# Kernel optimization log

Measured on AMD Instinct MI355X. Metric: run time of the kernel, lower is better.

Reference implementation:

```python
import jax, jax.numpy as jnp
import numpy as np

N, N2, N3 = 40000, 20000, 10000
E, E2, E3 = 640000, 320000, 160000
HEADS = 4
F_IN = 5


def _glorot(k, shape):
    lim = float(np.sqrt(6.0 / (shape[0] + shape[-1])))
    return jax.random.uniform(k, shape, jnp.float32, -lim, lim)


def setup_inputs() -> dict:
    key = jax.random.key(0)
    ks = jax.random.split(key, 40)
    inp = {}
    inp["x"] = jax.random.normal(ks[0], (N, F_IN), jnp.float32)
    inp["edge_index"] = jax.random.randint(ks[1], (2, E), 0, N)
    inp["edge_index2"] = jax.random.randint(ks[2], (2, E2), 0, N2)
    inp["edge_index3"] = jax.random.randint(ks[3], (2, E3), 0, N3)
    # graclus-style cluster maps; constructed surjective so no cluster is empty
    inp["cluster1"] = jax.random.permutation(ks[4], jnp.arange(N) % N2)
    inp["cluster2"] = jax.random.permutation(ks[5], jnp.arange(N2) % N3)
    dims = [(F_IN, 16), (16, 32), (32, 64), (64, 32), (64, 16)]
    i = 6
    for idx, (fi, fo) in enumerate(dims, 1):
        inp[f"cW{idx}"] = _glorot(ks[i], (fi, HEADS * fo)); i += 1
        inp[f"cU{idx}"] = _glorot(ks[i], (fi, HEADS)); i += 1
        inp[f"cc{idx}"] = jnp.zeros((HEADS,), jnp.float32)
        inp[f"cb{idx}"] = jnp.zeros((fo,), jnp.float32)
    inp["l1W"] = _glorot(ks[i], (32, 256)); i += 1
    inp["l1b"] = jnp.zeros((256,), jnp.float32)
    inp["l2W"] = _glorot(ks[i], (256, 6890)); i += 1
    inp["l2b"] = jnp.zeros((6890,), jnp.float32)
    inp["oW"] = _glorot(ks[i], (6890, 1)); i += 1
    inp["ob"] = jnp.zeros((1,), jnp.float32)
    return inp


def feast_conv(x, ei, W, U, c, b, n, fo):
    """PyG FeaStConv: self-loops, per-edge head-softmax attention, mean aggregation."""
    sl = jnp.arange(n)
    src = jnp.concatenate([ei[0], sl])  # message sources (x_j)
    dst = jnp.concatenate([ei[1], sl])  # aggregation targets (x_i)
    xs, xd = x[src], x[dst]
    q = jax.nn.softmax((xs - xd) @ U + c, axis=-1)          # [E+n, H]
    m = (xs @ W).reshape(-1, HEADS, fo)                      # [E+n, H, fo]
    msg = jnp.einsum('eh,eho->eo', q, m)                     # [E+n, fo]
    agg = jax.ops.segment_sum(msg, dst, num_segments=n)
    cnt = jax.ops.segment_sum(jnp.ones((dst.shape[0],), x.dtype), dst, num_segments=n)
    return agg / cnt[:, None] + b


def _forward(x, edge_index, edge_index2, edge_index3, cluster1, cluster2, p):
    x1 = jax.nn.relu(feast_conv(x, edge_index, p["cW1"], p["cU1"], p["cc1"], p["cb1"], N, 16))
    x2 = jax.ops.segment_max(x1, cluster1, num_segments=N2)                     # graclus max_pool
    x2 = jax.nn.relu(feast_conv(x2, edge_index2, p["cW2"], p["cU2"], p["cc2"], p["cb2"], N2, 32))
    x3 = jax.ops.segment_max(x2, cluster2, num_segments=N3)
    x3 = jax.nn.relu(feast_conv(x3, edge_index3, p["cW3"], p["cU3"], p["cc3"], p["cb3"], N3, 64))
    x3 = jax.nn.relu(feast_conv(x3, edge_index3, p["cW4"], p["cU4"], p["cc4"], p["cb4"], N3, 32))
    x3 = jnp.concatenate([x2, x3[cluster2]], axis=1)                            # [N2, 64] unpool+skip
    x3 = jax.nn.relu(feast_conv(x3, edge_index2, p["cW5"], p["cU5"], p["cc5"], p["cb5"], N2, 16))
    h = jnp.concatenate([x1, x3[cluster1]], axis=1)                             # [N, 32]
    h = jax.nn.relu(h @ p["l1W"] + p["l1b"])
    h = jax.nn.relu(h @ p["l2W"] + p["l2b"])                                   # [N, 6890]
    return jax.nn.sigmoid(h @ p["oW"] + p["ob"])                                # [N, 1]


def reference(x, edge_index, edge_index2, edge_index3, cluster1, cluster2,
              cW1, cU1, cc1, cb1, cW2, cU2, cc2, cb2, cW3, cU3, cc3, cb3,
              cW4, cU4, cc4, cb4, cW5, cU5, cc5, cb5, l1W, l1b, l2W, l2b, oW, ob):
    p = dict(cW1=cW1, cU1=cU1, cc1=cc1, cb1=cb1, cW2=cW2, cU2=cU2, cc2=cc2, cb2=cb2,
             cW3=cW3, cU3=cU3, cc3=cc3, cb3=cb3, cW4=cW4, cU4=cU4, cc4=cc4, cb4=cb4,
             cW5=cW5, cU5=cU5, cc5=cc5, cb5=cb5, l1W=l1W, l1b=l1b, l2W=l2W, l2b=l2b,
             oW=oW, ob=ob)
    return _forward(x, edge_index, edge_index2, edge_index3, cluster1, cluster2, p)
```

## Files before the change

### kernel.cpp

```cpp
#include <hip/hip_runtime.h>
#include <math.h>

#define N1  40000
#define NN2 20000
#define NN3 10000
#define EE1 640000
#define EE2 320000
#define EE3 160000
#define JPAD 6912
#define JREAL 6890
#define NTILE 432
#define CSPLIT 8
#define TPB (NTILE/CSPLIT)
#define NSTG (TPB/2)
#define NROWP 40192
#define NGRP 628
#define CAP 64

typedef __attribute__((ext_vector_type(8))) short short8;
typedef __attribute__((ext_vector_type(4))) float f32x4;

__device__ inline unsigned short f2bf(float f) {
  unsigned u = __float_as_uint(f);
  u += 0x7FFF + ((u >> 16) & 1);
  return (unsigned short)(u >> 16);
}

__global__ void k_matmulWU(const float* __restrict__ Xa, int fa,
                           const float* __restrict__ Xb, int fb,
                           const int* __restrict__ map,
                           const float* __restrict__ W, const float* __restrict__ U,
                           float* __restrict__ xW, float* __restrict__ xU,
                           int n, int co) {
  int ct = co + 4;
  int idx = blockIdx.x * 256 + threadIdx.x;
  if (idx >= n * ct) return;
  int row = idx / ct, col = idx - row * ct;
  const float* M;
  int stride;
  if (col < co) { M = W + col; stride = co; }
  else          { M = U + (col - co); stride = 4; }
  float s = 0.f;
  const float* ar = Xa + (size_t)row * fa;
  for (int k = 0; k < fa; ++k) s = fmaf(ar[k], M[(size_t)k * stride], s);
  if (Xb) {
    const float* br = Xb + (size_t)map[row] * fb;
    for (int k = 0; k < fb; ++k) s = fmaf(br[k], M[(size_t)(fa + k) * stride], s);
  }
  if (col < co) xW[(size_t)row * co + col] = s;
  else          xU[(size_t)row * 4 + (col - co)] = s;
}

__global__ void k_xU(const float* __restrict__ xin, const float* __restrict__ U,
                     float* __restrict__ xu, int n, int ci) {
  int idx = blockIdx.x * 256 + threadIdx.x;
  if (idx >= n * 4) return;
  int h = idx & 3, d = idx >> 2;
  const float* xr = xin + (size_t)d * ci;
  float s = 0.f;
  for (int k = 0; k < ci; ++k) s = fmaf(xr[k], U[k * 4 + h], s);
  xu[idx] = s;
}

__global__ void k_pad8(const float* __restrict__ x, float* __restrict__ x8) {
  int idx = blockIdx.x * 256 + threadIdx.x;
  if (idx >= N1 * 8) return;
  int d = idx >> 3, k = idx & 7;
  x8[idx] = (k < 5) ? x[d * 5 + k] : 0.f;
}

__global__ void k_build3(const int* __restrict__ ei1, const int* __restrict__ ei2,
                         const int* __restrict__ ei3,
                         int* __restrict__ c1, int* __restrict__ c2, int* __restrict__ c3,
                         int* __restrict__ s1, int* __restrict__ s2, int* __restrict__ s3) {
  int e = blockIdx.x * 256 + threadIdx.x;
  const int* ei; int* cnt; int* sl; int E;
  if (e < EE1) { ei = ei1; cnt = c1; sl = s1; E = EE1; }
  else {
    e -= EE1;
    if (e < EE2) { ei = ei2; cnt = c2; sl = s2; E = EE2; }
    else {
      e -= EE2;
      if (e >= EE3) return;
      ei = ei3; cnt = c3; sl = s3; E = EE3;
    }
  }
  int s = ei[e], d = ei[E + e];
  int pos = atomicAdd(&cnt[d], 1);
  if (pos < CAP) sl[(size_t)d * CAP + pos] = s;
}

__global__ void k_aggX(const int* __restrict__ cnt, const int* __restrict__ slots,
                       const float* __restrict__ xU, const f32x4* __restrict__ xin4,
                       int stride4, const float* __restrict__ c,
                       f32x4* __restrict__ agg4, int n, int ci4) {
  int idx = blockIdx.x * 256 + threadIdx.x;
  if (idx >= n * ci4 * 4) return;
  const int sp = idx & 3;
  int t = idx >> 2;
  const int cg = t % ci4, d = t / ci4;
  const float c0 = c[0], c1 = c[1], c2 = c[2], c3 = c[3];
  const f32x4 xd = ((const f32x4*)xU)[d];
  const int deg = min(cnt[d], CAP);
  const int jlo = (deg * sp) >> 2, jhi = (deg * (sp + 1)) >> 2;
  const int* sl = slots + (size_t)d * CAP;
  f32x4 acc[4];
#pragma unroll
  for (int e = 0; e < 4; ++e) acc[e] = (f32x4){0.f, 0.f, 0.f, 0.f};
  int j = jlo;
  for (; j + 2 <= jhi; j += 2) {
    int sA = sl[j], sB = sl[j + 1];
    f32x4 xsA = ((const f32x4*)xU)[sA];
    f32x4 xsB = ((const f32x4*)xU)[sB];
    f32x4 xvA = xin4[(size_t)sA * stride4 + cg];
    f32x4 xvB = xin4[(size_t)sB * stride4 + cg];
    float lA0 = xsA[0] - xd[0] + c0, lA1 = xsA[1] - xd[1] + c1;
    float lA2 = xsA[2] - xd[2] + c2, lA3 = xsA[3] - xd[3] + c3;
    float mxA = fmaxf(fmaxf(lA0, lA1), fmaxf(lA2, lA3));
    float qA0 = __expf(lA0 - mxA), qA1 = __expf(lA1 - mxA);
    float qA2 = __expf(lA2 - mxA), qA3 = __expf(lA3 - mxA);
    float ivA = 1.f / (qA0 + qA1 + qA2 + qA3);
    f32x4 qA = (f32x4){qA0 * ivA, qA1 * ivA, qA2 * ivA, qA3 * ivA};
    float lB0 = xsB[0] - xd[0] + c0, lB1 = xsB[1] - xd[1] + c1;
    float lB2 = xsB[2] - xd[2] + c2, lB3 = xsB[3] - xd[3] + c3;
    float mxB = fmaxf(fmaxf(lB0, lB1), fmaxf(lB2, lB3));
    float qB0 = __expf(lB0 - mxB), qB1 = __expf(lB1 - mxB);
    float qB2 = __expf(lB2 - mxB), qB3 = __expf(lB3 - mxB);
    float ivB = 1.f / (qB0 + qB1 + qB2 + qB3);
    f32x4 qB = (f32x4){qB0 * ivB, qB1 * ivB, qB2 * ivB, qB3 * ivB};
#pragma unroll
    for (int e = 0; e < 4; ++e) acc[e] += xvA[e] * qA + xvB[e] * qB;
  }
  if (j < jhi) {
    int s = sl[j];
    f32x4 xs = ((const f32x4*)xU)[s];
    f32x4 xv = xin4[(size_t)s * stride4 + cg];
    float l0 = xs[0] - xd[0] + c0, l1 = xs[1] - xd[1] + c1;
    float l2 = xs[2] - xd[2] + c2, l3 = xs[3] - xd[3] + c3;
    float mx = fmaxf(fmaxf(l0, l1), fmaxf(l2, l3));
    float q0 = __expf(l0 - mx), q1 = __expf(l1 - mx);
    float q2 = __expf(l2 - mx), q3 = __expf(l3 - mx);
    float iv = 1.f / (q0 + q1 + q2 + q3);
    f32x4 q = (f32x4){q0 * iv, q1 * iv, q2 * iv, q3 * iv};
#pragma unroll
    for (int e = 0; e < 4; ++e) acc[e] += xv[e] * q;
  }
#pragma unroll
  for (int e = 0; e < 4; ++e)
#pragma unroll
    for (int h = 0; h < 4; ++h) {
      acc[e][h] += __shfl_xor(acc[e][h], 1);
      acc[e][h] += __shfl_xor(acc[e][h], 2);
    }
  if (sp) return;
  {
    float mx = fmaxf(fmaxf(c0, c1), fmaxf(c2, c3));
    float q0 = __expf(c0 - mx), q1 = __expf(c1 - mx);
    float q2 = __expf(c2 - mx), q3 = __expf(c3 - mx);
    float iv = 1.f / (q0 + q1 + q2 + q3);
    f32x4 q = (f32x4){q0 * iv, q1 * iv, q2 * iv, q3 * iv};
    f32x4 xv = xin4[(size_t)d * stride4 + cg];
#pragma unroll
    for (int e = 0; e < 4; ++e) acc[e] += xv[e] * q;
  }
  f32x4* dst = agg4 + (size_t)d * (ci4 * 4) + cg * 4;
#pragma unroll
  for (int e = 0; e < 4; ++e) dst[e] = acc[e];
}

__global__ void k_postW(const f32x4* __restrict__ agg4, int aggstride, int kreal,
                        const float* __restrict__ W, const float* __restrict__ b,
                        const int* __restrict__ cnt, float* __restrict__ outp,
                        int n, int fo,
                        const int* __restrict__ pool_cl, int* __restrict__ pool_out) {
  int idx = blockIdx.x * 256 + threadIdx.x;
  if (idx >= n * fo) return;
  int o = idx % fo, d = idx / fo;
  const int co = 4 * fo;
  const f32x4* ar = agg4 + (size_t)d * aggstride;
  float acc = 0.f;
  for (int k = 0; k < kreal; ++k) {
    f32x4 f = ar[k];
    const float* wr = W + (size_t)k * co + o;
    acc += f[0] * wr[0] + f[1] * wr[fo] + f[2] * wr[2 * fo] + f[3] * wr[3 * fo];
  }
  int deg = min(cnt[d], CAP);
  float v = fmaxf(acc / (float)(deg + 1) + b[o], 0.f);
  outp[idx] = v;
  if (pool_cl)
    atomicMax((int*)&pool_out[(size_t)pool_cl[d] * fo + o], __float_as_int(v));
}

__global__ void k_attagg4(const int* __restrict__ cnt, const int* __restrict__ slots,
                          const float* __restrict__ xU, const float4* __restrict__ xW,
                          const float* __restrict__ c, const float4* __restrict__ b4,
                          float4* __restrict__ outp, int n, int fo4,
                          const int* __restrict__ pool_cl, int* __restrict__ pool_out) {
  int idx = blockIdx.x * 256 + threadIdx.x;
  if (idx >= n * fo4 * 4) return;
  const int sp = idx & 3;
  const int t = idx >> 2;
  const int d = t / fo4, og = t - d * fo4;
  const float c0 = c[0], c1 = c[1], c2 = c[2], c3 = c[3];
  const float4 xd = *(const float4*)&xU[(size_t)d * 4];
  const int deg = min(cnt[d], CAP);
  const int jlo = (deg * sp) >> 2;
  const int jhi = (deg * (sp + 1)) >> 2;
  const int* sl = slots + (size_t)d * CAP;
  float ax = 0.f, ay = 0.f, az = 0.f, aw = 0.f;
  int j = jlo;
  for (; j + 2 <= jhi; j += 2) {
    int sA = sl[j], sB = sl[j + 1];
    float4 xsA = *(const float4*)&xU[(size_t)sA * 4];
    float4 xsB = *(const float4*)&xU[(size_t)sB * 4];
    const float4* mA = xW + (size_t)sA * 4 * fo4 + og;
    const float4* mB = xW + (size_t)sB * 4 * fo4 + og;
    float4 a0 = mA[0], a1 = mA[fo4], a2 = mA[2 * fo4], a3 = mA[3 * fo4];
    float4 e0 = mB[0], e1 = mB[fo4], e2 = mB[2 * fo4], e3 = mB[3 * fo4];
    float lA0 = xsA.x - xd.x + c0, lA1 = xsA.y - xd.y + c1;
    float lA2 = xsA.z - xd.z + c2, lA3 = xsA.w - xd.w + c3;
    float mxA = fmaxf(fmaxf(lA0, lA1), fmaxf(lA2, lA3));
    float qA0 = __expf(lA0 - mxA), qA1 = __expf(lA1 - mxA);
    float qA2 = __expf(lA2 - mxA), qA3 = __expf(lA3 - mxA);
    float ivA = 1.f / (qA0 + qA1 + qA2 + qA3);
    qA0 *= ivA; qA1 *= ivA; qA2 *= ivA; qA3 *= ivA;
    float lB0 = xsB.x - xd.x + c0, lB1 = xsB.y - xd.y + c1;
    float lB2 = xsB.z - xd.z + c2, lB3 = xsB.w - xd.w + c3;
    float mxB = fmaxf(fmaxf(lB0, lB1), fmaxf(lB2, lB3));
    float qB0 = __expf(lB0 - mxB), qB1 = __expf(lB1 - mxB);
    float qB2 = __expf(lB2 - mxB), qB3 = __expf(lB3 - mxB);
    float ivB = 1.f / (qB0 + qB1 + qB2 + qB3);
    qB0 *= ivB; qB1 *= ivB; qB2 *= ivB; qB3 *= ivB;
    ax += qA0 * a0.x + qA1 * a1.x + qA2 * a2.x + qA3 * a3.x
        + qB0 * e0.x + qB1 * e1.x + qB2 * e2.x + qB3 * e3.x;
    ay += qA0 * a0.y + qA1 * a1.y + qA2 * a2.y + qA3 * a3.y
        + qB0 * e0.y + qB1 * e1.y + qB2 * e2.y + qB3 * e3.y;
    az += qA0 * a0.z + qA1 * a1.z + qA2 * a2.z + qA3 * a3.z
        + qB0 * e0.z + qB1 * e1.z + qB2 * e2.z + qB3 * e3.z;
    aw += qA0 * a0.w + qA1 * a1.w + qA2 * a2.w + qA3 * a3.w
        + qB0 * e0.w + qB1 * e1.w + qB2 * e2.w + qB3 * e3.w;
  }
  if (j < jhi) {
    int s = sl[j];
    float4 xs = *(const float4*)&xU[(size_t)s * 4];
    const float4* m = xW + (size_t)s * 4 * fo4 + og;
    float4 m0 = m[0], m1 = m[fo4], m2 = m[2 * fo4], m3 = m[3 * fo4];
    float l0 = xs.x - xd.x + c0, l1 = xs.y - xd.y + c1;
    float l2 = xs.z - xd.z + c2, l3 = xs.w - xd.w + c3;
    float mx = fmaxf(fmaxf(l0, l1), fmaxf(l2, l3));
    float q0 = __expf(l0 - mx), q1 = __expf(l1 - mx);
    float q2 = __expf(l2 - mx), q3 = __expf(l3 - mx);
    float inv = 1.f / (q0 + q1 + q2 + q3);
    q0 *= inv; q1 *= inv; q2 *= inv; q3 *= inv;
    ax += q0 * m0.x + q1 * m1.x + q2 * m2.x + q3 * m3.x;
    ay += q0 * m0.y + q1 * m1.y + q2 * m2.y + q3 * m3.y;
    az += q0 * m0.z + q1 * m1.z + q2 * m2.z + q3 * m3.z;
    aw += q0 * m0.w + q1 * m1.w + q2 * m2.w + q3 * m3.w;
  }
  ax += __shfl_xor(ax, 1); ay += __shfl_xor(ay, 1);
  az += __shfl_xor(az, 1); aw += __shfl_xor(aw, 1);
  ax += __shfl_xor(ax, 2); ay += __shfl_xor(ay, 2);
  az += __shfl_xor(az, 2); aw += __shfl_xor(aw, 2);
  if (sp) return;
  {
    float mx = fmaxf(fmaxf(c0, c1), fmaxf(c2, c3));
    float q0 = __expf(c0 - mx), q1 = __expf(c1 - mx);
    float q2 = __expf(c2 - mx), q3 = __expf(c3 - mx);
    float inv = 1.f / (q0 + q1 + q2 + q3);
    const float4* m = xW + (size_t)d * 4 * fo4 + og;
    float4 m0 = m[0], m1 = m[fo4], m2 = m[2 * fo4], m3 = m[3 * fo4];
    ax += (q0 * m0.x + q1 * m1.x + q2 * m2.x + q3 * m3.x) * inv;
    ay += (q0 * m0.y + q1 * m1.y + q2 * m2.y + q3 * m3.y) * inv;
    az += (q0 * m0.z + q1 * m1.z + q2 * m2.z + q3 * m3.z) * inv;
    aw += (q0 * m0.w + q1 * m1.w + q2 * m2.w + q3 * m3.w) * inv;
  }
  const float inv = 1.f / (float)(deg + 1);
  const float4 bb = b4[og];
  float4 v;
  v.x = fmaxf(ax * inv + bb.x, 0.f);
  v.y = fmaxf(ay * inv + bb.y, 0.f);
  v.z = fmaxf(az * inv + bb.z, 0.f);
  v.w = fmaxf(aw * inv + bb.w, 0.f);
  outp[(size_t)d * fo4 + og] = v;
  if (pool_cl) {
    int* po = pool_out + ((size_t)pool_cl[d] * fo4 + og) * 4;
    atomicMax(&po[0], __float_as_int(v.x));
    atomicMax(&po[1], __float_as_int(v.y));
    atomicMax(&po[2], __float_as_int(v.z));
    atomicMax(&po[3], __float_as_int(v.w));
  }
}

__global__ __launch_bounds__(256) void k_packB(
    const float* __restrict__ l2W, short8* __restrict__ Bp,
    const float* __restrict__ l2b, const float* __restrict__ oW,
    float* __restrict__ l2bp, float* __restrict__ oWp) {
  __shared__ float tile[32][65];
  const int bid = blockIdx.x, tid = threadIdx.x;
  if (bid < 27) {
    int j = bid * 256 + tid;
    l2bp[j] = (j < JREAL) ? l2b[j] : 0.f;
    oWp[j]  = (j < JREAL) ? oW[j]  : 0.f;
  }
  const int kg = bid / 108, jg = bid - kg * 108;
  const int k0 = kg * 32, j0 = jg * 64;
  const int kr = tid >> 6, jc = tid & 63;
  const int j = j0 + jc;
#pragma unroll
  for (int i = 0; i < 8; ++i) {
    int row = kr * 8 + i;
    tile[row][jc] = (j < JREAL) ? l2W[(size_t)(k0 + row) * JREAL + j] : 0.f;
  }
  __syncthreads();
  const int tt = tid >> 6, lane = tid & 63;
  short8 v;
#pragma unroll
  for (int i = 0; i < 8; ++i)
    v[i] = (short)f2bf(tile[((lane >> 4) << 3) + i][tt * 16 + (lane & 15)]);
  Bp[((size_t)(jg * 4 + tt) * 8 + kg) * 64 + lane] = v;
}

__global__ __launch_bounds__(256) void k_packh(
    const float* __restrict__ x1, const float* __restrict__ x5,
    const int* __restrict__ cl1, const float* __restrict__ l1W,
    const float* __restrict__ l1b, short8* __restrict__ Apack) {
  __shared__ float h1s[64][256];
  const int tid = threadIdx.x;
  const int row0 = blockIdx.x * 64;

  float wcol[32];
#pragma unroll
  for (int k = 0; k < 32; ++k) wcol[k] = l1W[k * 256 + tid];
  const float bt = l1b[tid];

  for (int r = 0; r < 64; ++r) {
    const int row = row0 + r;
    float s = bt;
    if (row < N1) {
      const float* a = x1 + (size_t)row * 16;
      const float* b = x5 + (size_t)cl1[row] * 16;
#pragma unroll
      for (int k = 0; k < 16; ++k) s = fmaf(a[k], wcol[k], s);
#pragma unroll
      for (int k = 0; k < 16; ++k) s = fmaf(b[k], wcol[16 + k], s);
    }
    h1s[r][tid ^ ((r & 7) << 3)] = fmaxf(s, 0.f);
  }
  __syncthreads();

#pragma unroll
  for (int j = 0; j < 8; ++j) {
    int s = j * 256 + tid;
    int l = s & 63, ks = (s >> 6) & 7, rb = s >> 9;
    int row = rb * 16 + (l & 15);
    int col0 = (ks * 32 + ((l >> 4) << 3)) ^ ((row & 7) << 3);
    const float* sp = &h1s[row][col0];
    short8 v;
#pragma unroll
    for (int i = 0; i < 8; ++i) v[i] = (short)f2bf(sp[i]);
    Apack[(size_t)blockIdx.x * 2048 + s] = v;
  }
}

__global__ __launch_bounds__(256, 2) void k_final2(
    const short8* __restrict__ Apack, const short8* __restrict__ Bp,
    const float* __restrict__ l2bp, const float* __restrict__ oWp,
    float* __restrict__ zbuf) {
  __shared__ short8 bufs[2][1024];
  const int tid = threadIdx.x, wid = tid >> 6, l = tid & 63;
  const int rg = blockIdx.x >> 3, cg = blockIdx.x & 7;
  const int lm = l & 15, lh = l >> 4;

  short8 af[4][8];
  {
    const short8* ap = Apack + (size_t)(rg * 4 + wid) * 2048 + l;
#pragma unroll
    for (int rb = 0; rb < 4; ++rb)
#pragma unroll
      for (int ks = 0; ks < 8; ++ks) af[rb][ks] = ap[rb * 512 + ks * 64];
  }

  const short8* bsrc = Bp + (size_t)cg * TPB * 512;
  short8 n0 = bsrc[tid], n1 = bsrc[256 + tid], n2 = bsrc[512 + tid], n3 = bsrc[768 + tid];
  bufs[0][tid] = n0; bufs[0][256 + tid] = n1;
  bufs[0][512 + tid] = n2; bufs[0][768 + tid] = n3;
  {
    const short8* p = bsrc + 1024;
    n0 = p[tid]; n1 = p[256 + tid]; n2 = p[512 + tid]; n3 = p[768 + tid];
  }
  asm volatile("s_waitcnt lgkmcnt(0)" ::: "memory");
  __builtin_amdgcn_s_barrier();
  asm volatile("" ::: "memory");

  float zp[4][4];
#pragma unroll
  for (int rb = 0; rb < 4; ++rb)
#pragma unroll
    for (int r = 0; r < 4; ++r) zp[rb][r] = 0.f;

  for (int st = 0; st < NSTG; ++st) {
    const int cur = st & 1;
    if (st + 1 < NSTG) {
      bufs[cur ^ 1][tid] = n0; bufs[cur ^ 1][256 + tid] = n1;
      bufs[cur ^ 1][512 + tid] = n2; bufs[cur ^ 1][768 + tid] = n3;
    }
    if (st + 2 < NSTG) {
      const short8* p = bsrc + (st + 2) * 1024;
      n0 = p[tid]; n1 = p[256 + tid]; n2 = p[512 + tid]; n3 = p[768 + tid];
    }
#pragma unroll
    for (int half = 0; half < 2; ++half) {
      short8 bfr[8];
#pragma unroll
      for (int ks = 0; ks < 8; ++ks) bfr[ks] = bufs[cur][half * 512 + ks * 64 + l];

      f32x4 acc[4];
#pragma unroll
      for (int rb = 0; rb < 4; ++rb) acc[rb] = (f32x4){0.f, 0.f, 0.f, 0.f};
      __builtin_amdgcn_s_setprio(1);
#pragma unroll
      for (int ks = 0; ks < 8; ++ks)
#pragma unroll
        for (int rb = 0; rb < 4; ++rb)
          acc[rb] = __builtin_amdgcn_mfma_f32_16x16x32_bf16(af[rb][ks], bfr[ks], acc[rb], 0, 0, 0);
      __builtin_amdgcn_s_setprio(0);

      const int j = (cg * TPB + st * 2 + half) * 16 + lm;
      const float lb = l2bp[j];
      const float ow = oWp[j];
#pragma unroll
      for (int rb = 0; rb < 4; ++rb)
#pragma unroll
        for (int r = 0; r < 4; ++r)
          zp[rb][r] += fmaxf(acc[rb][r] + lb, 0.f) * ow;
    }
    asm volatile("s_waitcnt lgkmcnt(0)" ::: "memory");
    __builtin_amdgcn_s_barrier();
    asm volatile("" ::: "memory");
  }

#pragma unroll
  for (int m = 1; m < 16; m <<= 1)
#pragma unroll
    for (int rb = 0; rb < 4; ++rb)
#pragma unroll
      for (int r = 0; r < 4; ++r)
        zp[rb][r] += __shfl_xor(zp[rb][r], m);

  if (lm == 0) {
    const int rbase = rg * 256 + wid * 64 + lh * 4;
#pragma unroll
    for (int rb = 0; rb < 4; ++rb)
#pragma unroll
      for (int r = 0; r < 4; ++r)
        atomicAdd(&zbuf[rbase + rb * 16 + r], zp[rb][r]);
  }
}

__global__ void k_sigm(const float* __restrict__ zbuf, const float* __restrict__ ob,
                       float* __restrict__ out) {
  int i = blockIdx.x * 256 + threadIdx.x;
  if (i >= N1) return;
  out[i] = 1.f / (1.f + expf(-(zbuf[i] + ob[0])));
}

static void run_conv(const float* xa, int fa, const float* xb, int fb, const int* gmap,
                     const int* cnt, const int* slots, int n, int fo,
                     const float* W, const float* U, const float* c, const float* b,
                     float* outp, float* xW, float* xU,
                     const int* pool_cl, int* pool_out, hipStream_t stream) {
  int co = 4 * fo;
  k_matmulWU<<<(n * (co + 4) + 255) / 256, 256, 0, stream>>>(xa, fa, xb, fb, gmap,
                                                             W, U, xW, xU, n, co);
  k_attagg4<<<(n * (fo / 4) * 4 + 255) / 256, 256, 0, stream>>>(
      cnt, slots, xU, (const float4*)xW, c, (const float4*)b, (float4*)outp, n, fo / 4,
      pool_cl, pool_out);
}

static void run_conv_agg(const float* xin, const float* xin_pad4, int stride4, int ci,
                         int ci4, const int* cnt, const int* slots, int n, int fo,
                         const float* W, const float* U, const float* c, const float* b,
                         float* outp, float* xu, float* aggbuf,
                         const int* pool_cl, int* pool_out, hipStream_t stream) {
  k_xU<<<(n * 4 + 255) / 256, 256, 0, stream>>>(xin, U, xu, n, ci);
  k_aggX<<<(n * ci4 * 4 + 255) / 256, 256, 0, stream>>>(
      cnt, slots, xu, (const f32x4*)xin_pad4, stride4, c, (f32x4*)aggbuf, n, ci4);
  k_postW<<<(n * fo + 255) / 256, 256, 0, stream>>>(
      (const f32x4*)aggbuf, ci4 * 4, ci, W, b, cnt, outp, n, fo, pool_cl, pool_out);
}

extern "C" void kernel_launch(void* const* d_in, const int* in_sizes, int n_in,
                              void* d_out, int out_size, void* d_ws, size_t ws_size,
                              hipStream_t stream) {
  const float* x   = (const float*)d_in[0];
  const int* ei1   = (const int*)d_in[1];
  const int* ei2   = (const int*)d_in[2];
  const int* ei3   = (const int*)d_in[3];
  const int* cl1   = (const int*)d_in[4];
  const int* cl2   = (const int*)d_in[5];
  const float* cW1 = (const float*)d_in[6],  *cU1 = (const float*)d_in[7],
             * cc1 = (const float*)d_in[8],  *cb1 = (const float*)d_in[9];
  const float* cW2 = (const float*)d_in[10], *cU2 = (const float*)d_in[11],
             * cc2 = (const float*)d_in[12], *cb2 = (const float*)d_in[13];
  const float* cW3 = (const float*)d_in[14], *cU3 = (const float*)d_in[15],
             * cc3 = (const float*)d_in[16], *cb3 = (const float*)d_in[17];
  const float* cW4 = (const float*)d_in[18], *cU4 = (const float*)d_in[19],
             * cc4 = (const float*)d_in[20], *cb4 = (const float*)d_in[21];
  const float* cW5 = (const float*)d_in[22], *cU5 = (const float*)d_in[23],
             * cc5 = (const float*)d_in[24], *cb5 = (const float*)d_in[25];
  const float* l1W = (const float*)d_in[26], *l1b = (const float*)d_in[27];
  const float* l2W = (const float*)d_in[28], *l2b = (const float*)d_in[29];
  const float* oW  = (const float*)d_in[30], *ob  = (const float*)d_in[31];

  float* ws = (float*)d_ws;
  float* x2p  = ws + 0;
  float* x3p  = ws + 320000;
  float* zbuf = ws + 640000;
  int*  cnt1  = (int*)(ws + 680192);
  int*  cnt2  = (int*)(ws + 720192);
  int*  cnt3  = (int*)(ws + 740192);
  int*  sl1   = (int*)(ws + 750192);
  int*  sl2   = (int*)(ws + 3310192);
  int*  sl3   = (int*)(ws + 4590192);
  float* x3a  = ws + 5230192;
  float* x3b  = ws + 5870192;
  float* x1   = ws + 6190192;
  float* x2   = ws + 6830192;
  float* x5   = ws + 7470192;
  short8* Bp  = (short8*)(ws + 7790192);
  float* l2bp = ws + 8674928;
  float* oWp  = ws + 8681840;
  float* xW   = ws + 8688752;
  float* xu   = ws + 11248752;
  float* x8   = ws + 11408752;
  float* aggbuf = ws + 11728752;
  short8* Apack = (short8*)(ws + 750192);

  hipMemsetAsync(ws, 0, 750192 * sizeof(float), stream);
  k_packB<<<864, 256, 0, stream>>>(l2W, Bp, l2b, oW, l2bp, oWp);

  const int ET = EE1 + EE2 + EE3;
  k_build3<<<(ET + 255) / 256, 256, 0, stream>>>(ei1, ei2, ei3, cnt1, cnt2, cnt3,
                                                 sl1, sl2, sl3);
  k_pad8<<<(N1 * 8 + 255) / 256, 256, 0, stream>>>(x, x8);

  run_conv_agg(x, x8, 2, 5, 2, cnt1, sl1, N1, 16, cW1, cU1, cc1, cb1,
               x1, xu, aggbuf, cl1, (int*)x2p, stream);
  run_conv_agg(x2p, x2p, 4, 16, 4, cnt2, sl2, NN2, 32, cW2, cU2, cc2, cb2,
               x2, xu, aggbuf, cl2, (int*)x3p, stream);
  run_conv_agg(x3p, x3p, 8, 32, 8, cnt3, sl3, NN3, 64, cW3, cU3, cc3, cb3,
               x3a, xu, aggbuf, nullptr, nullptr, stream);
  run_conv(x3a, 64, nullptr, 0, nullptr, cnt3, sl3, NN3, 32,
           cW4, cU4, cc4, cb4, x3b, xW, xu, nullptr, nullptr, stream);
  run_conv(x2, 32, x3b, 32, cl2, cnt2, sl2, NN2, 16,
           cW5, cU5, cc5, cb5, x5, xW, xu, nullptr, nullptr, stream);

  k_packh<<<NGRP, 256, 0, stream>>>(x1, x5, cl1, l1W, l1b, Apack);
  k_final2<<<(NROWP / 256) * CSPLIT, 256, 0, stream>>>(Apack, Bp, l2bp, oWp, zbuf);
  k_sigm<<<(N1 + 255) / 256, 256, 0, stream>>>(zbuf, ob, (float*)d_out);
}
```

Baseline: 487.4 us.

## Fuse prep kernels, unroll aggregation by four, widen final GEMM stages

Merges edge-slot building, input padding and the first-layer attention projection into a single prep kernel, removing two launches. Unrolls the neighbor aggregation loop to four edges per iteration with a shared softmax helper, which exposes more independent gathers. In the final bf16 MFMA GEMM it reduces the column split from 8 to 6 and doubles the per-stage B tile held in LDS and registers, trading fewer blocks and more register and LDS pressure for fewer pipeline stages.

```diff
diff --git a/kernel.cpp b/kernel.cpp
--- a/kernel.cpp
+++ b/kernel.cpp
@@ -7,12 +7,13 @@
 #define EE1 640000
 #define EE2 320000
 #define EE3 160000
+#define ET  (EE1 + EE2 + EE3)
 #define JPAD 6912
 #define JREAL 6890
 #define NTILE 432
-#define CSPLIT 8
+#define CSPLIT 6
 #define TPB (NTILE/CSPLIT)
-#define NSTG (TPB/2)
+#define NSTG (TPB/4)
 #define NROWP 40192
 #define NGRP 628
 #define CAP 64
@@ -24,6 +25,16 @@
   unsigned u = __float_as_uint(f);
   u += 0x7FFF + ((u >> 16) & 1);
   return (unsigned short)(u >> 16);
+}
+
+__device__ inline f32x4 qsoft(f32x4 xs, f32x4 xd, float c0, float c1, float c2, float c3) {
+  float l0 = xs[0] - xd[0] + c0, l1 = xs[1] - xd[1] + c1;
+  float l2 = xs[2] - xd[2] + c2, l3 = xs[3] - xd[3] + c3;
+  float mx = fmaxf(fmaxf(l0, l1), fmaxf(l2, l3));
+  float q0 = __expf(l0 - mx), q1 = __expf(l1 - mx);
+  float q2 = __expf(l2 - mx), q3 = __expf(l3 - mx);
+  float iv = 1.f / (q0 + q1 + q2 + q3);
+  return (f32x4){q0 * iv, q1 * iv, q2 * iv, q3 * iv};
 }
 
 __global__ void k_matmulWU(const float* __restrict__ Xa, int fa,
@@ -62,32 +73,42 @@
   xu[idx] = s;
 }
 
-__global__ void k_pad8(const float* __restrict__ x, float* __restrict__ x8) {
-  int idx = blockIdx.x * 256 + threadIdx.x;
-  if (idx >= N1 * 8) return;
-  int d = idx >> 3, k = idx & 7;
-  x8[idx] = (k < 5) ? x[d * 5 + k] : 0.f;
-}
-
-__global__ void k_build3(const int* __restrict__ ei1, const int* __restrict__ ei2,
-                         const int* __restrict__ ei3,
-                         int* __restrict__ c1, int* __restrict__ c2, int* __restrict__ c3,
-                         int* __restrict__ s1, int* __restrict__ s2, int* __restrict__ s3) {
-  int e = blockIdx.x * 256 + threadIdx.x;
-  const int* ei; int* cnt; int* sl; int E;
-  if (e < EE1) { ei = ei1; cnt = c1; sl = s1; E = EE1; }
-  else {
-    e -= EE1;
-    if (e < EE2) { ei = ei2; cnt = c2; sl = s2; E = EE2; }
+__global__ void k_prep(const int* __restrict__ ei1, const int* __restrict__ ei2,
+                       const int* __restrict__ ei3,
+                       int* __restrict__ c1, int* __restrict__ c2, int* __restrict__ c3,
+                       int* __restrict__ s1, int* __restrict__ s2, int* __restrict__ s3,
+                       const float* __restrict__ x, float* __restrict__ x8,
+                       const float* __restrict__ U1, float* __restrict__ xu1) {
+  int i = blockIdx.x * 256 + threadIdx.x;
+  if (i < ET) {
+    int e = i;
+    const int* ei; int* cnt; int* sl; int E;
+    if (e < EE1) { ei = ei1; cnt = c1; sl = s1; E = EE1; }
     else {
-      e -= EE2;
-      if (e >= EE3) return;
-      ei = ei3; cnt = c3; sl = s3; E = EE3;
+      e -= EE1;
+      if (e < EE2) { ei = ei2; cnt = c2; sl = s2; E = EE2; }
+      else { e -= EE2; ei = ei3; cnt = c3; sl = s3; E = EE3; }
     }
-  }
-  int s = ei[e], d = ei[E + e];
-  int pos = atomicAdd(&cnt[d], 1);
-  if (pos < CAP) sl[(size_t)d * CAP + pos] = s;
+    int s = ei[e], d = ei[E + e];
+    int pos = atomicAdd(&cnt[d], 1);
+    if (pos < CAP) sl[(size_t)d * CAP + pos] = s;
+    return;
+  }
+  i -= ET;
+  if (i < N1 * 8) {
+    int d = i >> 3, k = i & 7;
+    x8[i] = (k < 5) ? x[d * 5 + k] : 0.f;
+    return;
+  }
+  i -= N1 * 8;
+  if (i < N1 * 4) {
+    int h = i & 3, d = i >> 2;
+    const float* xr = x + (size_t)d * 5;
+    float s = 0.f;
+#pragma unroll
+    for (int k = 0; k < 5; ++k) s = fmaf(xr[k], U1[k * 4 + h], s);
+    xu1[i] = s;
+  }
 }
 
 __global__ void k_aggX(const int* __restrict__ cnt, const int* __restrict__ slots,
@@ -100,7 +121,8 @@
   int t = idx >> 2;
   const int cg = t % ci4, d = t / ci4;
   const float c0 = c[0], c1 = c[1], c2 = c[2], c3 = c[3];
-  const f32x4 xd = ((const f32x4*)xU)[d];
+  const f32x4* XU4 = (const f32x4*)xU;
+  const f32x4 xd = XU4[d];
   const int deg = min(cnt[d], CAP);
   const int jlo = (deg * sp) >> 2, jhi = (deg * (sp + 1)) >> 2;
   const int* sl = slots + (size_t)d * CAP;
@@ -108,42 +130,28 @@
 #pragma unroll
   for (int e = 0; e < 4; ++e) acc[e] = (f32x4){0.f, 0.f, 0.f, 0.f};
   int j = jlo;
-  for (; j + 2 <= jhi; j += 2) {
-    int sA = sl[j], sB = sl[j + 1];
-    f32x4 xsA = ((const f32x4*)xU)[sA];
-    f32x4 xsB = ((const f32x4*)xU)[sB];
-    f32x4 xvA = xin4[(size_t)sA * stride4 + cg];
-    f32x4 xvB = xin4[(size_t)sB * stride4 + cg];
-    float lA0 = xsA[0] - xd[0] + c0, lA1 = xsA[1] - xd[1] + c1;
-    float lA2 = xsA[2] - xd[2] + c2, lA3 = xsA[3] - xd[3] + c3;
-    float mxA = fmaxf(fmaxf(lA0, lA1), fmaxf(lA2, lA3));
-    float qA0 = __expf(lA0 - mxA), qA1 = __expf(lA1 - mxA);
-    float qA2 = __expf(lA2 - mxA), qA3 = __expf(lA3 - mxA);
-    float ivA = 1.f / (qA0 + qA1 + qA2 + qA3);
-    f32x4 qA = (f32x4){qA0 * ivA, qA1 * ivA, qA2 * ivA, qA3 * ivA};
-    float lB0 = xsB[0] - xd[0] + c0, lB1 = xsB[1] - xd[1] + c1;
-    float lB2 = xsB[2] - xd[2] + c2, lB3 = xsB[3] - xd[3] + c3;
-    float mxB = fmaxf(fmaxf(lB0, lB1), fmaxf(lB2, lB3));
-    float qB0 = __expf(lB0 - mxB), qB1 = __expf(lB1 - mxB);
-    float qB2 = __expf(lB2 - mxB), qB3 = __expf(lB3 - mxB);
-    float ivB = 1.f / (qB0 + qB1 + qB2 + qB3);
-    f32x4 qB = (f32x4){qB0 * ivB, qB1 * ivB, qB2 * ivB, qB3 * ivB};
-#pragma unroll
-    for (int e = 0; e < 4; ++e) acc[e] += xvA[e] * qA + xvB[e] * qB;
-  }
-  if (j < jhi) {
+  for (; j + 4 <= jhi; j += 4) {
+    int s0 = sl[j], s1 = sl[j + 1], s2 = sl[j + 2], s3 = sl[j + 3];
+    f32x4 u0 = XU4[s0], u1 = XU4[s1], u2 = XU4[s2], u3 = XU4[s3];
+    f32x4 v0 = xin4[(size_t)s0 * stride4 + cg];
+    f32x4 v1 = xin4[(size_t)s1 * stride4 + cg];
+    f32x4 v2 = xin4[(size_t)s2 * stride4 + cg];
+    f32x4 v3 = xin4[(size_t)s3 * stride4 + cg];
+    f32x4 q0 = qsoft(u0, xd, c0, c1, c2, c3);
+    f32x4 q1 = qsoft(u1, xd, c0, c1, c2, c3);
+    f32x4 q2 = qsoft(u2, xd, c0, c1, c2, c3);
+    f32x4 q3 = qsoft(u3, xd, c0, c1, c2, c3);
+#pragma unroll
+    for (int e = 0; e < 4; ++e)
+      acc[e] += v0[e] * q0 + v1[e] * q1 + v2[e] * q2 + v3[e] * q3;
+  }
+  for (; j < jhi; ++j) {
     int s = sl[j];
-    f32x4 xs = ((const f32x4*)xU)[s];
-    f32x4 xv = xin4[(size_t)s * stride4 + cg];
-    float l0 = xs[0] - xd[0] + c0, l1 = xs[1] - xd[1] + c1;
-    float l2 = xs[2] - xd[2] + c2, l3 = xs[3] - xd[3] + c3;
-    float mx = fmaxf(fmaxf(l0, l1), fmaxf(l2, l3));
-    float q0 = __expf(l0 - mx), q1 = __expf(l1 - mx);
-    float q2 = __expf(l2 - mx), q3 = __expf(l3 - mx);
-    float iv = 1.f / (q0 + q1 + q2 + q3);
-    f32x4 q = (f32x4){q0 * iv, q1 * iv, q2 * iv, q3 * iv};
-#pragma unroll
-    for (int e = 0; e < 4; ++e) acc[e] += xv[e] * q;
+    f32x4 u = XU4[s];
+    f32x4 v = xin4[(size_t)s * stride4 + cg];
+    f32x4 q = qsoft(u, xd, c0, c1, c2, c3);
+#pragma unroll
+    for (int e = 0; e < 4; ++e) acc[e] += v[e] * q;
   }
 #pragma unroll
   for (int e = 0; e < 4; ++e)
@@ -366,9 +374,9 @@
     const short8* __restrict__ Apack, const short8* __restrict__ Bp,
     const float* __restrict__ l2bp, const float* __restrict__ oWp,
     float* __restrict__ zbuf) {
-  __shared__ short8 bufs[2][1024];
+  __shared__ short8 bufs[2][2048];
   const int tid = threadIdx.x, wid = tid >> 6, l = tid & 63;
-  const int rg = blockIdx.x >> 3, cg = blockIdx.x & 7;
+  const int rg = blockIdx.x / CSPLIT, cg = blockIdx.x % CSPLIT;
   const int lm = l & 15, lh = l >> 4;
 
   short8 af[4][8];
@@ -381,13 +389,14 @@
   }
 
   const short8* bsrc = Bp + (size_t)cg * TPB * 512;
-  short8 n0 = bsrc[tid], n1 = bsrc[256 + tid], n2 = bsrc[512 + tid], n3 = bsrc[768 + tid];
-  bufs[0][tid] = n0; bufs[0][256 + tid] = n1;
-  bufs[0][512 + tid] = n2; bufs[0][768 + tid] = n3;
-  {
-    const short8* p = bsrc + 1024;
-    n0 = p[tid]; n1 = p[256 + tid]; n2 = p[512 + tid]; n3 = p[768 + tid];
-  }
+  short8 nreg[8];
+#pragma unroll
+  for (int i = 0; i < 8; ++i) {
+    short8 v = bsrc[i * 256 + tid];
+    bufs[0][i * 256 + tid] = v;
+  }
+#pragma unroll
+  for (int i = 0; i < 8; ++i) nreg[i] = bsrc[2048 + i * 256 + tid];
   asm volatile("s_waitcnt lgkmcnt(0)" ::: "memory");
   __builtin_amdgcn_s_barrier();
   asm volatile("" ::: "memory");
@@ -401,18 +410,19 @@
   for (int st = 0; st < NSTG; ++st) {
     const int cur = st & 1;
     if (st + 1 < NSTG) {
-      bufs[cur ^ 1][tid] = n0; bufs[cur ^ 1][256 + tid] = n1;
-      bufs[cur ^ 1][512 + tid] = n2; bufs[cur ^ 1][768 + tid] = n3;
+#pragma unroll
+      for (int i = 0; i < 8; ++i) bufs[cur ^ 1][i * 256 + tid] = nreg[i];
     }
     if (st + 2 < NSTG) {
-      const short8* p = bsrc + (st + 2) * 1024;
-      n0 = p[tid]; n1 = p[256 + tid]; n2 = p[512 + tid]; n3 = p[768 + tid];
+      const short8* p = bsrc + (st + 2) * 2048;
+#pragma unroll
+      for (int i = 0; i < 8; ++i) nreg[i] = p[i * 256 + tid];
     }
 #pragma unroll
-    for (int half = 0; half < 2; ++half) {
+    for (int q = 0; q < 4; ++q) {
       short8 bfr[8];
 #pragma unroll
-      for (int ks = 0; ks < 8; ++ks) bfr[ks] = bufs[cur][half * 512 + ks * 64 + l];
+      for (int ks = 0; ks < 8; ++ks) bfr[ks] = bufs[cur][q * 512 + ks * 64 + l];
 
       f32x4 acc[4];
 #pragma unroll
@@ -425,7 +435,7 @@
           acc[rb] = __builtin_amdgcn_mfma_f32_16x16x32_bf16(af[rb][ks], bfr[ks], acc[rb], 0, 0, 0);
       __builtin_amdgcn_s_setprio(0);
 
-      const int j = (cg * TPB + st * 2 + half) * 16 + lm;
+      const int j = (cg * TPB + st * 4 + q) * 16 + lm;
       const float lb = l2bp[j];
       const float ow = oWp[j];
 #pragma unroll
@@ -477,12 +487,11 @@
       pool_cl, pool_out);
 }
 
-static void run_conv_agg(const float* xin, const float* xin_pad4, int stride4, int ci,
-                         int ci4, const int* cnt, const int* slots, int n, int fo,
-                         const float* W, const float* U, const float* c, const float* b,
-                         float* outp, float* xu, float* aggbuf,
+static void run_conv_agg(const float* xin_pad4, int stride4, int ci, int ci4,
+                         const int* cnt, const int* slots, int n, int fo,
+                         const float* W, const float* c, const float* b,
+                         float* outp, const float* xu, float* aggbuf,
                          const int* pool_cl, int* pool_out, hipStream_t stream) {
-  k_xU<<<(n * 4 + 255) / 256, 256, 0, stream>>>(xin, U, xu, n, ci);
   k_aggX<<<(n * ci4 * 4 + 255) / 256, 256, 0, stream>>>(
       cnt, slots, xu, (const f32x4*)xin_pad4, stride4, c, (f32x4*)aggbuf, n, ci4);
   k_postW<<<(n * fo + 255) / 256, 256, 0, stream>>>(
@@ -539,16 +548,16 @@
   hipMemsetAsync(ws, 0, 750192 * sizeof(float), stream);
   k_packB<<<864, 256, 0, stream>>>(l2W, Bp, l2b, oW, l2bp, oWp);
 
-  const int ET = EE1 + EE2 + EE3;
-  k_build3<<<(ET + 255) / 256, 256, 0, stream>>>(ei1, ei2, ei3, cnt1, cnt2, cnt3,
-                                                 sl1, sl2, sl3);
-  k_pad8<<<(N1 * 8 + 255) / 256, 256, 0, stream>>>(x, x8);
-
-  run_conv_agg(x, x8, 2, 5, 2, cnt1, sl1, N1, 16, cW1, cU1, cc1, cb1,
+  k_prep<<<(ET + N1 * 8 + N1 * 4 + 255) / 256, 256, 0, stream>>>(
+      ei1, ei2, ei3, cnt1, cnt2, cnt3, sl1, sl2, sl3, x, x8, cU1, xu);
+
+  run_conv_agg(x8, 2, 5, 2, cnt1, sl1, N1, 16, cW1, cc1, cb1,
                x1, xu, aggbuf, cl1, (int*)x2p, stream);
-  run_conv_agg(x2p, x2p, 4, 16, 4, cnt2, sl2, NN2, 32, cW2, cU2, cc2, cb2,
+  k_xU<<<(NN2 * 4 + 255) / 256, 256, 0, stream>>>(x2p, cU2, xu, NN2, 16);
+  run_conv_agg(x2p, 4, 16, 4, cnt2, sl2, NN2, 32, cW2, cc2, cb2,
                x2, xu, aggbuf, cl2, (int*)x3p, stream);
-  run_conv_agg(x3p, x3p, 8, 32, 8, cnt3, sl3, NN3, 64, cW3, cU3, cc3, cb3,
+  k_xU<<<(NN3 * 4 + 255) / 256, 256, 0, stream>>>(x3p, cU3, xu, NN3, 32);
+  run_conv_agg(x3p, 8, 32, 8, cnt3, sl3, NN3, 64, cW3, cc3, cb3,
                x3a, xu, aggbuf, nullptr, nullptr, stream);
   run_conv(x3a, 64, nullptr, 0, nullptr, cnt3, sl3, NN3, 32,
            cW4, cU4, cc4, cb4, x3b, xW, xu, nullptr, nullptr, stream);
```

New measurement: 627.9 us. +28.8%, slower.
